# Optimization experiments

Hardware: AMD Instinct MI355X
Metric: run time of the kernel (lower is better)

## Reference

```python
import jax, jax.numpy as jnp
import numpy as np

B, S, D, H = 2, 2048, 1024, 16
DK = D // H


def setup_inputs() -> dict:
    key = jax.random.key(0)
    ks = jax.random.split(key, 11)
    scale = 1.0 / np.sqrt(D)
    inp = {
        "query": jax.random.normal(ks[0], (B, S, D), dtype=jnp.float32),
        "key": jax.random.normal(ks[1], (B, S, D), dtype=jnp.float32),
        "value": jax.random.normal(ks[2], (B, S, D), dtype=jnp.float32),
        "Wq": jax.random.normal(ks[3], (D, D), dtype=jnp.float32) * scale,
        "bq": jnp.zeros((D,), dtype=jnp.float32),
        "Wk": jax.random.normal(ks[4], (D, D), dtype=jnp.float32) * scale,
        "bk": jnp.zeros((D,), dtype=jnp.float32),
        "Wv": jax.random.normal(ks[5], (D, D), dtype=jnp.float32) * scale,
        "bv": jnp.zeros((D,), dtype=jnp.float32),
        "Wo": jax.random.normal(ks[6], (D, D), dtype=jnp.float32) * scale,
        "bo": jnp.zeros((D,), dtype=jnp.float32),
    }
    return inp


def _split_heads(x):
    # [B,S,D] -> [B,H,S,DK]
    b, s, _ = x.shape
    return x.reshape(b, s, H, DK).transpose(0, 2, 1, 3)


def reference(query, key, value, Wq, bq, Wk, bk, Wv, bv, Wo, bo):
    q = _split_heads(query @ Wq.T + bq)
    k = _split_heads(key @ Wk.T + bk)
    v = _split_heads(value @ Wv.T + bv)
    # scaled dot-product attention: [B,H,S,S]
    scores = jnp.einsum("bhqd,bhkd->bhqk", q, k) / np.sqrt(DK).astype(np.float32)
    attn = jax.nn.softmax(scores, axis=-1)  # stable max-subtract softmax, same math
    ctx = jnp.einsum("bhqk,bhkd->bhqd", attn, v)  # [B,H,S,DK]
    ctx = ctx.transpose(0, 2, 1, 3).reshape(query.shape[0], -1, H * DK)
    return ctx @ Wo.T + bo
```

## Files before the change

### kernel.cpp

```cpp
#include <hip/hip_runtime.h>
#include <math.h>

constexpr int NB = 2;
constexpr int NS = 2048;
constexpr int ND = 1024;
constexpr int NH = 16;
constexpr int NDK = 64;

typedef __attribute__((ext_vector_type(8))) short short8;
typedef __attribute__((ext_vector_type(4))) float floatx4;

__device__ inline unsigned short f2bf(float x) {
    unsigned u = __builtin_bit_cast(unsigned, x);
    u += 0x7fffu + ((u >> 16) & 1u);
    return (unsigned short)(u >> 16);
}

#define GLOAD_LDS16(g, l) __builtin_amdgcn_global_load_lds( \
    (const __attribute__((address_space(1))) void*)(g),     \
    (__attribute__((address_space(3))) void*)(l), 16, 0, 0)

#define QSCALE 0.18033688f

__global__ __launch_bounds__(256) void cvt_all(
    const float* __restrict__ s0, const float* __restrict__ s1,
    const float* __restrict__ s2, const float* __restrict__ s3,
    const float* __restrict__ s4, const float* __restrict__ s5,
    const float* __restrict__ s6,
    unsigned short* __restrict__ d0, unsigned short* __restrict__ d1,
    unsigned short* __restrict__ d2, unsigned short* __restrict__ d3,
    unsigned short* __restrict__ d4, unsigned short* __restrict__ d5,
    unsigned short* __restrict__ d6)
{
    const int y = blockIdx.y;
    const float* srcs[7] = {s0, s1, s2, s3, s4, s5, s6};
    unsigned short* dsts[7] = {d0, d1, d2, d3, d4, d5, d6};
    const int nel = (y < 3) ? NB * NS * ND : ND * ND;
    int i = (blockIdx.x * 256 + threadIdx.x) * 8;
    if (i >= nel) return;
    const float* s = srcs[y];
    unsigned short* d = dsts[y];
    float4 a = *(const float4*)(s + i);
    float4 b = *(const float4*)(s + i + 4);
    unsigned short t[8] = {f2bf(a.x), f2bf(a.y), f2bf(a.z), f2bf(a.w),
                           f2bf(b.x), f2bf(b.y), f2bf(b.z), f2bf(b.w)};
    *(uint4*)(d + i) = *(uint4*)t;
}

__global__ __launch_bounds__(256) void gemm_qkv(
    const unsigned short* __restrict__ Xq, const unsigned short* __restrict__ Xk,
    const unsigned short* __restrict__ Xv,
    const unsigned short* __restrict__ Wq, const unsigned short* __restrict__ Wk,
    const unsigned short* __restrict__ Wv,
    const float* __restrict__ bq, const float* __restrict__ bk,
    const float* __restrict__ bv,
    unsigned short* __restrict__ Cq, unsigned short* __restrict__ Ck,
    unsigned short* __restrict__ Cv)
{
    __shared__ unsigned short As[128 * 32];
    __shared__ unsigned short Bs[128 * 32];
    const int tid = threadIdx.x, w = tid >> 6, lane = tid & 63;
    const int lo = lane & 15, quad = lane >> 4;
    const int bid = blockIdx.x;
    const int seg = bid >> 8;
    const int wi  = bid & 255;
    const int K = ND;

    int bm, bn;
    const unsigned short *A, *Bw;
    const float* bias;
    if (seg == 2)      { bn = wi & 31; bm = wi >> 5; A = Wv; Bw = Xv; bias = bv; }
    else if (seg == 1) { bn = wi & 7;  bm = wi >> 3; A = Xk; Bw = Wk; bias = bk; }
    else               { bn = wi & 7;  bm = wi >> 3; A = Xq; Bw = Wq; bias = bq; }

    const int wm = (w >> 1) * 64, wn = (w & 1) * 64;

    const int srow = tid >> 2;
    const int sch = (tid & 3) ^ (srow & 3);
    const unsigned short* Ag0 = A + (size_t)(bm * 128 + srow) * K + sch * 8;
    const unsigned short* Ag1 = Ag0 + (size_t)64 * K;
    const unsigned short* Bg0 = Bw + (size_t)(bn * 128 + srow) * K + sch * 8;
    const unsigned short* Bg1 = Bg0 + (size_t)64 * K;
    unsigned short* AsD0 = As + tid * 8;
    unsigned short* AsD1 = As + (tid + 256) * 8;
    unsigned short* BsD0 = Bs + tid * 8;
    unsigned short* BsD1 = Bs + (tid + 256) * 8;

    floatx4 acc[4][4];
    #pragma unroll
    for (int i = 0; i < 4; ++i)
        #pragma unroll
        for (int j = 0; j < 4; ++j) acc[i][j] = (floatx4){0.f, 0.f, 0.f, 0.f};

    const int rpos = (quad ^ (lo & 3)) * 8;

    for (int k0 = 0; k0 < K; k0 += 32) {
        GLOAD_LDS16(Ag0 + k0, AsD0);
        GLOAD_LDS16(Ag1 + k0, AsD1);
        GLOAD_LDS16(Bg0 + k0, BsD0);
        GLOAD_LDS16(Bg1 + k0, BsD1);
        __syncthreads();

        short8 af[4], bf[4];
        #pragma unroll
        for (int i = 0; i < 4; ++i)
            af[i] = *(const short8*)(As + (wm + i * 16 + lo) * 32 + rpos);
        #pragma unroll
        for (int j = 0; j < 4; ++j)
            bf[j] = *(const short8*)(Bs + (wn + j * 16 + lo) * 32 + rpos);

        #pragma unroll
        for (int i = 0; i < 4; ++i)
            #pragma unroll
            for (int j = 0; j < 4; ++j)
                acc[i][j] = __builtin_amdgcn_mfma_f32_16x16x32_bf16(af[i], bf[j], acc[i][j], 0, 0, 0);
        __syncthreads();
    }

    if (seg < 2) {
        unsigned short* C = seg ? Ck : Cq;
        const float scale = seg ? 1.f : QSCALE;
        #pragma unroll
        for (int j = 0; j < 4; ++j) {
            const int col = bn * 128 + wn + j * 16 + lo;
            const float bb = bias[col];
            #pragma unroll
            for (int i = 0; i < 4; ++i)
                #pragma unroll
                for (int r = 0; r < 4; ++r) {
                    const int row = bm * 128 + wm + i * 16 + quad * 4 + r;
                    C[(size_t)row * ND + col] = f2bf((acc[i][j][r] + bb) * scale);
                }
        }
    } else {
        #pragma unroll
        for (int i = 0; i < 4; ++i)
            #pragma unroll
            for (int r = 0; r < 4; ++r) {
                const int row = bm * 128 + wm + i * 16 + quad * 4 + r;
                const float bb = bias[row];
                #pragma unroll
                for (int j = 0; j < 4; ++j) {
                    const int col = bn * 128 + wn + j * 16 + lo;
                    const int b = col >> 11, s = col & (NS - 1);
                    Cv[(size_t)(b * ND + row) * NS + s] = f2bf(acc[i][j][r] + bb);
                }
            }
    }
}

__global__ __launch_bounds__(256) void gemm_o(
    const unsigned short* __restrict__ A, const unsigned short* __restrict__ Bw,
    const float* __restrict__ bias, float* __restrict__ Cout)
{
    __shared__ unsigned short As[64 * 64];
    __shared__ unsigned short Bs[128 * 64];
    const int tid = threadIdx.x, w = tid >> 6, lane = tid & 63;
    const int lo = lane & 15, quad = lane >> 4;
    const int bn = blockIdx.x, bm = blockIdx.y;
    const int K = ND;
    const int wm = (w >> 1) * 32, wn = (w & 1) * 64;

    const int ar0 = tid >> 3,            ag0 = (tid & 7) ^ (ar0 & 7);
    const int ar1 = (tid + 256) >> 3,    ag1 = (tid & 7) ^ (ar1 & 7);
    const unsigned short* Ag0 = A + (size_t)(bm * 64 + ar0) * K + ag0 * 8;
    const unsigned short* Ag1 = A + (size_t)(bm * 64 + ar1) * K + ag1 * 8;
    unsigned short* AsD0 = As + tid * 8;
    unsigned short* AsD1 = As + (tid + 256) * 8;

    const unsigned short* Bg[4];
    unsigned short* BsD[4];
    #pragma unroll
    for (int p = 0; p < 4; ++p) {
        int c = tid + 256 * p, r = c >> 3, g = (c & 7) ^ (r & 7);
        Bg[p] = Bw + (size_t)(bn * 128 + r) * K + g * 8;
        BsD[p] = Bs + c * 8;
    }

    floatx4 acc[2][4];
    #pragma unroll
    for (int i = 0; i < 2; ++i)
        #pragma unroll
        for (int j = 0; j < 4; ++j) acc[i][j] = (floatx4){0.f, 0.f, 0.f, 0.f};

    for (int k0 = 0; k0 < K; k0 += 64) {
        GLOAD_LDS16(Ag0 + k0, AsD0);
        GLOAD_LDS16(Ag1 + k0, AsD1);
        #pragma unroll
        for (int p = 0; p < 4; ++p) GLOAD_LDS16(Bg[p] + k0, BsD[p]);
        __syncthreads();

        #pragma unroll
        for (int s = 0; s < 2; ++s) {
            const int pos = ((s * 4 + quad) ^ (lo & 7)) * 8;
            short8 af[2], bf[4];
            #pragma unroll
            for (int i = 0; i < 2; ++i)
                af[i] = *(const short8*)(As + (wm + i * 16 + lo) * 64 + pos);
            #pragma unroll
            for (int j = 0; j < 4; ++j)
                bf[j] = *(const short8*)(Bs + (wn + j * 16 + lo) * 64 + pos);
            #pragma unroll
            for (int i = 0; i < 2; ++i)
                #pragma unroll
                for (int j = 0; j < 4; ++j)
                    acc[i][j] = __builtin_amdgcn_mfma_f32_16x16x32_bf16(af[i], bf[j], acc[i][j], 0, 0, 0);
        }
        __syncthreads();
    }

    #pragma unroll
    for (int j = 0; j < 4; ++j) {
        const int col = bn * 128 + wn + j * 16 + lo;
        const float bb = bias[col];
        #pragma unroll
        for (int i = 0; i < 2; ++i)
            #pragma unroll
            for (int r = 0; r < 4; ++r) {
                const int row = bm * 64 + wm + i * 16 + quad * 4 + r;
                Cout[(size_t)row * ND + col] = acc[i][j][r] + bb;
            }
    }
}

constexpr int PRS = 72;

__global__ __launch_bounds__(256, 4) void attn_mfma(
    const unsigned short* __restrict__ qb,
    const unsigned short* __restrict__ kb,
    const unsigned short* __restrict__ vt,
    float* __restrict__ cacc0, float* __restrict__ cacc1,
    float* __restrict__ lbuf)
{
    __shared__ unsigned short Ks[64 * 64];
    __shared__ unsigned short Vs[64 * 64];
    __shared__ unsigned short Pt[4][32 * PRS];

    const int tid = threadIdx.x, w = tid >> 6, lane = tid & 63;
    const int lo = lane & 15, quad = lane >> 4;
    const int qgrp = blockIdx.x;
    const int ksp  = blockIdx.y;
    const int bh   = blockIdx.z;
    const int b = bh >> 4, h = bh & 15;
    const int q0 = qgrp * 128 + w * 32;

    short8 qf[2][2];
    #pragma unroll
    for (int qt = 0; qt < 2; ++qt) {
        const unsigned short* qrow =
            qb + (size_t)(b * NS + q0 + qt * 16 + lo) * ND + h * NDK + quad * 8;
        qf[qt][0] = *(const short8*)(qrow);
        qf[qt][1] = *(const short8*)(qrow + 32);
    }

    const int c0 = tid, c1 = tid + 256;
    const int r0 = c0 >> 3, g0 = (c0 & 7) ^ (r0 & 7);
    const int r1 = c1 >> 3, g1 = (c1 & 7) ^ (r1 & 7);
    const unsigned short* Ksrc0 = kb + (size_t)(b * NS + r0) * ND + h * NDK + g0 * 8;
    const unsigned short* Ksrc1 = kb + (size_t)(b * NS + r1) * ND + h * NDK + g1 * 8;
    const unsigned short* Vsrc0 = vt + (size_t)(bh * NDK + r0) * NS + g0 * 8;
    const unsigned short* Vsrc1 = vt + (size_t)(bh * NDK + r1) * NS + g1 * 8;
    unsigned short* Kd0 = Ks + c0 * 8;
    unsigned short* Kd1 = Ks + c1 * 8;
    unsigned short* Vd0 = Vs + c0 * 8;
    unsigned short* Vd1 = Vs + c1 * 8;

    floatx4 acc[2][4], lacc[2];
    #pragma unroll
    for (int qt = 0; qt < 2; ++qt) {
        lacc[qt] = (floatx4){0.f, 0.f, 0.f, 0.f};
        #pragma unroll
        for (int cb = 0; cb < 4; ++cb) acc[qt][cb] = (floatx4){0.f, 0.f, 0.f, 0.f};
    }

    const short8 ones = {0x3F80, 0x3F80, 0x3F80, 0x3F80,
                         0x3F80, 0x3F80, 0x3F80, 0x3F80};
    unsigned short* pw = &Pt[w][0];
    const int pos0 = (quad ^ (lo & 7)) * 8;
    const int pos1 = ((4 + quad) ^ (lo & 7)) * 8;

    for (int key0 = ksp * 1024; key0 < ksp * 1024 + 1024; key0 += 64) {
        GLOAD_LDS16(Ksrc0 + (size_t)key0 * ND, Kd0);
        GLOAD_LDS16(Ksrc1 + (size_t)key0 * ND, Kd1);
        GLOAD_LDS16(Vsrc0 + key0, Vd0);
        GLOAD_LDS16(Vsrc1 + key0, Vd1);
        __syncthreads();

        floatx4 s[2][4];
        #pragma unroll
        for (int t = 0; t < 4; ++t) {
            const int rw = (t * 16 + lo) * 64;
            const short8 kf0 = *(const short8*)(Ks + rw + pos0);
            const short8 kf1 = *(const short8*)(Ks + rw + pos1);
            #pragma unroll
            for (int qt = 0; qt < 2; ++qt) {
                s[qt][t] = __builtin_amdgcn_mfma_f32_16x16x32_bf16(
                    kf0, qf[qt][0], (floatx4){0.f, 0.f, 0.f, 0.f}, 0, 0, 0);
                s[qt][t] = __builtin_amdgcn_mfma_f32_16x16x32_bf16(
                    kf1, qf[qt][1], s[qt][t], 0, 0, 0);
            }
        }

        #pragma unroll
        for (int qt = 0; qt < 2; ++qt)
            #pragma unroll
            for (int t = 0; t < 4; ++t) {
                unsigned u0 = __builtin_bit_cast(unsigned, __builtin_amdgcn_exp2f(s[qt][t][0]));
                unsigned u1 = __builtin_bit_cast(unsigned, __builtin_amdgcn_exp2f(s[qt][t][1]));
                unsigned u2 = __builtin_bit_cast(unsigned, __builtin_amdgcn_exp2f(s[qt][t][2]));
                unsigned u3 = __builtin_bit_cast(unsigned, __builtin_amdgcn_exp2f(s[qt][t][3]));
                uint2 pk = {(u0 >> 16) | (u1 & 0xFFFF0000u),
                            (u2 >> 16) | (u3 & 0xFFFF0000u)};
                *(uint2*)(pw + (qt * 16 + lo) * PRS + t * 16 + quad * 4) = pk;
            }

        short8 pf[2][2];
        #pragma unroll
        for (int qt = 0; qt < 2; ++qt) {
            pf[qt][0] = *(const short8*)(pw + (qt * 16 + lo) * PRS + quad * 8);
            pf[qt][1] = *(const short8*)(pw + (qt * 16 + lo) * PRS + 32 + quad * 8);
            lacc[qt] = __builtin_amdgcn_mfma_f32_16x16x32_bf16(pf[qt][0], ones, lacc[qt], 0, 0, 0);
            lacc[qt] = __builtin_amdgcn_mfma_f32_16x16x32_bf16(pf[qt][1], ones, lacc[qt], 0, 0, 0);
        }

        #pragma unroll
        for (int cb = 0; cb < 4; ++cb) {
            const int rw = (cb * 16 + lo) * 64;
            const short8 vf0 = *(const short8*)(Vs + rw + pos0);
            const short8 vf1 = *(const short8*)(Vs + rw + pos1);
            #pragma unroll
            for (int qt = 0; qt < 2; ++qt) {
                acc[qt][cb] = __builtin_amdgcn_mfma_f32_16x16x32_bf16(pf[qt][0], vf0, acc[qt][cb], 0, 0, 0);
                acc[qt][cb] = __builtin_amdgcn_mfma_f32_16x16x32_bf16(pf[qt][1], vf1, acc[qt][cb], 0, 0, 0);
            }
        }
        __syncthreads();
    }

    float* ca = ksp ? cacc1 : cacc0;
    float* lb = lbuf + (size_t)ksp * (NB * NH * NS);
    #pragma unroll
    for (int qt = 0; qt < 2; ++qt) {
        #pragma unroll
        for (int cb = 0; cb < 4; ++cb)
            #pragma unroll
            for (int r = 0; r < 4; ++r) {
                size_t off = (size_t)(b * NS + q0 + qt * 16 + quad * 4 + r) * ND
                           + h * NDK + cb * 16 + lo;
                ca[off] = acc[qt][cb][r];
            }
        if (lo == 0)
            #pragma unroll
            for (int r = 0; r < 4; ++r)
                lb[(size_t)bh * NS + q0 + qt * 16 + quad * 4 + r] = lacc[qt][r];
    }
}

__global__ __launch_bounds__(256) void divide_ctx(
    const float* __restrict__ cacc0, const float* __restrict__ cacc1,
    const float* __restrict__ lbuf, unsigned short* __restrict__ ctx)
{
    int idx = blockIdx.x * 256 + threadIdx.x;
    int base = idx * 8;
    int row = base >> 10;
    int col = base & 1023;
    int b = row >> 11, sq = row & 2047, h = col >> 6;
    size_t li = (size_t)((b << 4) + h) * NS + sq;
    float inv = 1.f / (lbuf[li] + lbuf[li + (size_t)NB * NH * NS]);
    float4 a0 = *(const float4*)(cacc0 + base);
    float4 a1 = *(const float4*)(cacc0 + base + 4);
    float4 c0 = *(const float4*)(cacc1 + base);
    float4 c1 = *(const float4*)(cacc1 + base + 4);
    unsigned short o[8] = {
        f2bf((a0.x + c0.x) * inv), f2bf((a0.y + c0.y) * inv),
        f2bf((a0.z + c0.z) * inv), f2bf((a0.w + c0.w) * inv),
        f2bf((a1.x + c1.x) * inv), f2bf((a1.y + c1.y) * inv),
        f2bf((a1.z + c1.z) * inv), f2bf((a1.w + c1.w) * inv)};
    *(uint4*)(ctx + base) = *(uint4*)o;
}

extern "C" void kernel_launch(void* const* d_in, const int* in_sizes, int n_in,
                              void* d_out, int out_size, void* d_ws, size_t ws_size,
                              hipStream_t stream)
{
    const float* query = (const float*)d_in[0];
    const float* key   = (const float*)d_in[1];
    const float* value = (const float*)d_in[2];
    const float* Wq    = (const float*)d_in[3];
    const float* bq    = (const float*)d_in[4];
    const float* Wk    = (const float*)d_in[5];
    const float* bk    = (const float*)d_in[6];
    const float* Wv    = (const float*)d_in[7];
    const float* bv    = (const float*)d_in[8];
    const float* Wo    = (const float*)d_in[9];
    const float* bo    = (const float*)d_in[10];
    float* out = (float*)d_out;

    const size_t n  = (size_t)NB * NS * ND;
    const size_t nw = (size_t)ND * ND;

    unsigned short* X0   = (unsigned short*)d_ws;
    unsigned short* X1   = X0 + n;
    unsigned short* X2   = X1 + n;
    unsigned short* W0   = X2 + n;
    unsigned short* W1   = W0 + nw;
    unsigned short* W2   = W1 + nw;
    unsigned short* W3   = W2 + nw;
    unsigned short* qbuf = W3 + nw;
    unsigned short* kbuf = qbuf + n;
    unsigned short* vtb  = kbuf + n;
    float* cacc1 = (float*)(vtb + n);
    float* lbuf  = cacc1 + n;
    float* cacc0 = (float*)X1;
    unsigned short* ctxb = qbuf;

    const int M = NB * NS;

    cvt_all<<<dim3((int)(n / 2048), 7), 256, 0, stream>>>(
        query, key, value, Wq, Wk, Wv, Wo, X0, X1, X2, W0, W1, W2, W3);

    gemm_qkv<<<768, 256, 0, stream>>>(X0, X1, X2, W0, W1, W2,
                                      bq, bk, bv, qbuf, kbuf, vtb);

    attn_mfma<<<dim3(NS / 128, 2, NB * NH), 256, 0, stream>>>(
        qbuf, kbuf, vtb, cacc0, cacc1, lbuf);

    divide_ctx<<<(int)(n / 8 / 256), 256, 0, stream>>>(cacc0, cacc1, lbuf, ctxb);

    gemm_o<<<dim3(ND / 128, M / 64), 256, 0, stream>>>(ctxb, W3, bo, out);
}
```

Baseline: 234.4 us.

## Fuse fp32-to-bf16 conversion into GEMMs and fold context normalization into output GEMM

Removes the standalone conversion kernel by having the QKV and output GEMMs load fp32 operands through registers and convert to bf16 when writing to shared memory, using a register prefetch of the next K tile. It also removes the divide_ctx kernel: the output GEMM now reads both split-K context partials and the softmax denominators directly, sums and normalizes them, then converts to bf16 on the fly. This cuts two launches and the intermediate bf16 round trips through global memory. In exchange the GEMMs read twice as many bytes per tile, and the output GEMM re-reads the partials once per column block. The async global-to-LDS loads are replaced by register staging, which adds VALU work and register pressure.

```diff
diff --git a/kernel.cpp b/kernel.cpp
--- a/kernel.cpp
+++ b/kernel.cpp
@@ -16,42 +16,23 @@
     return (unsigned short)(u >> 16);
 }
 
+__device__ inline uint4 pack8(float4 a, float4 b) {
+    unsigned short t[8] = {f2bf(a.x), f2bf(a.y), f2bf(a.z), f2bf(a.w),
+                           f2bf(b.x), f2bf(b.y), f2bf(b.z), f2bf(b.w)};
+    return *(uint4*)t;
+}
+
 #define GLOAD_LDS16(g, l) __builtin_amdgcn_global_load_lds( \
     (const __attribute__((address_space(1))) void*)(g),     \
     (__attribute__((address_space(3))) void*)(l), 16, 0, 0)
 
 #define QSCALE 0.18033688f
 
-__global__ __launch_bounds__(256) void cvt_all(
-    const float* __restrict__ s0, const float* __restrict__ s1,
-    const float* __restrict__ s2, const float* __restrict__ s3,
-    const float* __restrict__ s4, const float* __restrict__ s5,
-    const float* __restrict__ s6,
-    unsigned short* __restrict__ d0, unsigned short* __restrict__ d1,
-    unsigned short* __restrict__ d2, unsigned short* __restrict__ d3,
-    unsigned short* __restrict__ d4, unsigned short* __restrict__ d5,
-    unsigned short* __restrict__ d6)
-{
-    const int y = blockIdx.y;
-    const float* srcs[7] = {s0, s1, s2, s3, s4, s5, s6};
-    unsigned short* dsts[7] = {d0, d1, d2, d3, d4, d5, d6};
-    const int nel = (y < 3) ? NB * NS * ND : ND * ND;
-    int i = (blockIdx.x * 256 + threadIdx.x) * 8;
-    if (i >= nel) return;
-    const float* s = srcs[y];
-    unsigned short* d = dsts[y];
-    float4 a = *(const float4*)(s + i);
-    float4 b = *(const float4*)(s + i + 4);
-    unsigned short t[8] = {f2bf(a.x), f2bf(a.y), f2bf(a.z), f2bf(a.w),
-                           f2bf(b.x), f2bf(b.y), f2bf(b.z), f2bf(b.w)};
-    *(uint4*)(d + i) = *(uint4*)t;
-}
-
 __global__ __launch_bounds__(256) void gemm_qkv(
-    const unsigned short* __restrict__ Xq, const unsigned short* __restrict__ Xk,
-    const unsigned short* __restrict__ Xv,
-    const unsigned short* __restrict__ Wq, const unsigned short* __restrict__ Wk,
-    const unsigned short* __restrict__ Wv,
+    const float* __restrict__ Xq, const float* __restrict__ Xk,
+    const float* __restrict__ Xv,
+    const float* __restrict__ Wq, const float* __restrict__ Wk,
+    const float* __restrict__ Wv,
     const float* __restrict__ bq, const float* __restrict__ bk,
     const float* __restrict__ bv,
     unsigned short* __restrict__ Cq, unsigned short* __restrict__ Ck,
@@ -67,8 +48,7 @@
     const int K = ND;
 
     int bm, bn;
-    const unsigned short *A, *Bw;
-    const float* bias;
+    const float *A, *Bw, *bias;
     if (seg == 2)      { bn = wi & 31; bm = wi >> 5; A = Wv; Bw = Xv; bias = bv; }
     else if (seg == 1) { bn = wi & 7;  bm = wi >> 3; A = Xk; Bw = Wk; bias = bk; }
     else               { bn = wi & 7;  bm = wi >> 3; A = Xq; Bw = Wq; bias = bq; }
@@ -77,10 +57,10 @@
 
     const int srow = tid >> 2;
     const int sch = (tid & 3) ^ (srow & 3);
-    const unsigned short* Ag0 = A + (size_t)(bm * 128 + srow) * K + sch * 8;
-    const unsigned short* Ag1 = Ag0 + (size_t)64 * K;
-    const unsigned short* Bg0 = Bw + (size_t)(bn * 128 + srow) * K + sch * 8;
-    const unsigned short* Bg1 = Bg0 + (size_t)64 * K;
+    const float* Ag0 = A + (size_t)(bm * 128 + srow) * K + sch * 8;
+    const float* Ag1 = Ag0 + (size_t)64 * K;
+    const float* Bg0 = Bw + (size_t)(bn * 128 + srow) * K + sch * 8;
+    const float* Bg1 = Bg0 + (size_t)64 * K;
     unsigned short* AsD0 = As + tid * 8;
     unsigned short* AsD1 = As + (tid + 256) * 8;
     unsigned short* BsD0 = Bs + tid * 8;
@@ -94,12 +74,27 @@
 
     const int rpos = (quad ^ (lo & 3)) * 8;
 
+    float4 ra[4], rb[4];
+    ra[0] = *(const float4*)(Ag0);     ra[1] = *(const float4*)(Ag0 + 4);
+    ra[2] = *(const float4*)(Ag1);     ra[3] = *(const float4*)(Ag1 + 4);
+    rb[0] = *(const float4*)(Bg0);     rb[1] = *(const float4*)(Bg0 + 4);
+    rb[2] = *(const float4*)(Bg1);     rb[3] = *(const float4*)(Bg1 + 4);
+
     for (int k0 = 0; k0 < K; k0 += 32) {
-        GLOAD_LDS16(Ag0 + k0, AsD0);
-        GLOAD_LDS16(Ag1 + k0, AsD1);
-        GLOAD_LDS16(Bg0 + k0, BsD0);
-        GLOAD_LDS16(Bg1 + k0, BsD1);
-        __syncthreads();
+        __syncthreads();
+        *(uint4*)AsD0 = pack8(ra[0], ra[1]);
+        *(uint4*)AsD1 = pack8(ra[2], ra[3]);
+        *(uint4*)BsD0 = pack8(rb[0], rb[1]);
+        *(uint4*)BsD1 = pack8(rb[2], rb[3]);
+        __syncthreads();
+
+        const int kn = k0 + 32;
+        if (kn < K) {
+            ra[0] = *(const float4*)(Ag0 + kn); ra[1] = *(const float4*)(Ag0 + kn + 4);
+            ra[2] = *(const float4*)(Ag1 + kn); ra[3] = *(const float4*)(Ag1 + kn + 4);
+            rb[0] = *(const float4*)(Bg0 + kn); rb[1] = *(const float4*)(Bg0 + kn + 4);
+            rb[2] = *(const float4*)(Bg1 + kn); rb[3] = *(const float4*)(Bg1 + kn + 4);
+        }
 
         short8 af[4], bf[4];
         #pragma unroll
@@ -114,7 +109,6 @@
             #pragma unroll
             for (int j = 0; j < 4; ++j)
                 acc[i][j] = __builtin_amdgcn_mfma_f32_16x16x32_bf16(af[i], bf[j], acc[i][j], 0, 0, 0);
-        __syncthreads();
     }
 
     if (seg < 2) {
@@ -145,80 +139,6 @@
                     const int b = col >> 11, s = col & (NS - 1);
                     Cv[(size_t)(b * ND + row) * NS + s] = f2bf(acc[i][j][r] + bb);
                 }
-            }
-    }
-}
-
-__global__ __launch_bounds__(256) void gemm_o(
-    const unsigned short* __restrict__ A, const unsigned short* __restrict__ Bw,
-    const float* __restrict__ bias, float* __restrict__ Cout)
-{
-    __shared__ unsigned short As[64 * 64];
-    __shared__ unsigned short Bs[128 * 64];
-    const int tid = threadIdx.x, w = tid >> 6, lane = tid & 63;
-    const int lo = lane & 15, quad = lane >> 4;
-    const int bn = blockIdx.x, bm = blockIdx.y;
-    const int K = ND;
-    const int wm = (w >> 1) * 32, wn = (w & 1) * 64;
-
-    const int ar0 = tid >> 3,            ag0 = (tid & 7) ^ (ar0 & 7);
-    const int ar1 = (tid + 256) >> 3,    ag1 = (tid & 7) ^ (ar1 & 7);
-    const unsigned short* Ag0 = A + (size_t)(bm * 64 + ar0) * K + ag0 * 8;
-    const unsigned short* Ag1 = A + (size_t)(bm * 64 + ar1) * K + ag1 * 8;
-    unsigned short* AsD0 = As + tid * 8;
-    unsigned short* AsD1 = As + (tid + 256) * 8;
-
-    const unsigned short* Bg[4];
-    unsigned short* BsD[4];
-    #pragma unroll
-    for (int p = 0; p < 4; ++p) {
-        int c = tid + 256 * p, r = c >> 3, g = (c & 7) ^ (r & 7);
-        Bg[p] = Bw + (size_t)(bn * 128 + r) * K + g * 8;
-        BsD[p] = Bs + c * 8;
-    }
-
-    floatx4 acc[2][4];
-    #pragma unroll
-    for (int i = 0; i < 2; ++i)
-        #pragma unroll
-        for (int j = 0; j < 4; ++j) acc[i][j] = (floatx4){0.f, 0.f, 0.f, 0.f};
-
-    for (int k0 = 0; k0 < K; k0 += 64) {
-        GLOAD_LDS16(Ag0 + k0, AsD0);
-        GLOAD_LDS16(Ag1 + k0, AsD1);
-        #pragma unroll
-        for (int p = 0; p < 4; ++p) GLOAD_LDS16(Bg[p] + k0, BsD[p]);
-        __syncthreads();
-
-        #pragma unroll
-        for (int s = 0; s < 2; ++s) {
-            const int pos = ((s * 4 + quad) ^ (lo & 7)) * 8;
-            short8 af[2], bf[4];
-            #pragma unroll
-            for (int i = 0; i < 2; ++i)
-                af[i] = *(const short8*)(As + (wm + i * 16 + lo) * 64 + pos);
-            #pragma unroll
-            for (int j = 0; j < 4; ++j)
-                bf[j] = *(const short8*)(Bs + (wn + j * 16 + lo) * 64 + pos);
-            #pragma unroll
-            for (int i = 0; i < 2; ++i)
-                #pragma unroll
-                for (int j = 0; j < 4; ++j)
-                    acc[i][j] = __builtin_amdgcn_mfma_f32_16x16x32_bf16(af[i], bf[j], acc[i][j], 0, 0, 0);
-        }
-        __syncthreads();
-    }
-
-    #pragma unroll
-    for (int j = 0; j < 4; ++j) {
-        const int col = bn * 128 + wn + j * 16 + lo;
-        const float bb = bias[col];
-        #pragma unroll
-        for (int i = 0; i < 2; ++i)
-            #pragma unroll
-            for (int r = 0; r < 4; ++r) {
-                const int row = bm * 64 + wm + i * 16 + quad * 4 + r;
-                Cout[(size_t)row * ND + col] = acc[i][j][r] + bb;
             }
     }
 }
@@ -356,27 +276,130 @@
     }
 }
 
-__global__ __launch_bounds__(256) void divide_ctx(
+__global__ __launch_bounds__(256) void gemm_o(
     const float* __restrict__ cacc0, const float* __restrict__ cacc1,
-    const float* __restrict__ lbuf, unsigned short* __restrict__ ctx)
+    const float* __restrict__ lbuf, const float* __restrict__ Bw,
+    const float* __restrict__ bias, float* __restrict__ Cout)
 {
-    int idx = blockIdx.x * 256 + threadIdx.x;
-    int base = idx * 8;
-    int row = base >> 10;
-    int col = base & 1023;
-    int b = row >> 11, sq = row & 2047, h = col >> 6;
-    size_t li = (size_t)((b << 4) + h) * NS + sq;
-    float inv = 1.f / (lbuf[li] + lbuf[li + (size_t)NB * NH * NS]);
-    float4 a0 = *(const float4*)(cacc0 + base);
-    float4 a1 = *(const float4*)(cacc0 + base + 4);
-    float4 c0 = *(const float4*)(cacc1 + base);
-    float4 c1 = *(const float4*)(cacc1 + base + 4);
-    unsigned short o[8] = {
-        f2bf((a0.x + c0.x) * inv), f2bf((a0.y + c0.y) * inv),
-        f2bf((a0.z + c0.z) * inv), f2bf((a0.w + c0.w) * inv),
-        f2bf((a1.x + c1.x) * inv), f2bf((a1.y + c1.y) * inv),
-        f2bf((a1.z + c1.z) * inv), f2bf((a1.w + c1.w) * inv)};
-    *(uint4*)(ctx + base) = *(uint4*)o;
+    __shared__ unsigned short As[64 * 64];
+    __shared__ unsigned short Bs[128 * 64];
+    const int tid = threadIdx.x, w = tid >> 6, lane = tid & 63;
+    const int lo = lane & 15, quad = lane >> 4;
+    const int bn = blockIdx.x, bm = blockIdx.y;
+    const int K = ND;
+    const int wm = (w >> 1) * 32, wn = (w & 1) * 64;
+    const size_t LHALF = (size_t)NB * NH * NS;
+
+    const int ar = tid >> 3;
+    const int ag = (tid & 7) ^ (ar & 7);
+    const int tok0 = bm * 64 + ar, tok1 = tok0 + 32;
+    const float* A00 = cacc0 + (size_t)tok0 * ND + ag * 8;
+    const float* A01 = cacc1 + (size_t)tok0 * ND + ag * 8;
+    const float* A10 = cacc0 + (size_t)tok1 * ND + ag * 8;
+    const float* A11 = cacc1 + (size_t)tok1 * ND + ag * 8;
+    const size_t lb0 = (size_t)((tok0 >> 11) << 4) * NS + (tok0 & (NS - 1));
+    const size_t lb1 = (size_t)((tok1 >> 11) << 4) * NS + (tok1 & (NS - 1));
+    unsigned short* AsD0 = As + tid * 8;
+    unsigned short* AsD1 = As + (tid + 256) * 8;
+
+    const float* Bg[4];
+    unsigned short* BsD[4];
+    #pragma unroll
+    for (int p = 0; p < 4; ++p) {
+        int c = tid + 256 * p, r = c >> 3, g = (c & 7) ^ (r & 7);
+        Bg[p] = Bw + (size_t)(bn * 128 + r) * K + g * 8;
+        BsD[p] = Bs + c * 8;
+    }
+
+    floatx4 acc[2][4];
+    #pragma unroll
+    for (int i = 0; i < 2; ++i)
+        #pragma unroll
+        for (int j = 0; j < 4; ++j) acc[i][j] = (floatx4){0.f, 0.f, 0.f, 0.f};
+
+    float4 ra[8], rb[8];
+    float lv0, lv1;
+    {
+        ra[0] = *(const float4*)(A00);     ra[1] = *(const float4*)(A00 + 4);
+        ra[2] = *(const float4*)(A01);     ra[3] = *(const float4*)(A01 + 4);
+        ra[4] = *(const float4*)(A10);     ra[5] = *(const float4*)(A10 + 4);
+        ra[6] = *(const float4*)(A11);     ra[7] = *(const float4*)(A11 + 4);
+        #pragma unroll
+        for (int p = 0; p < 4; ++p) {
+            rb[2 * p]     = *(const float4*)(Bg[p]);
+            rb[2 * p + 1] = *(const float4*)(Bg[p] + 4);
+        }
+        lv0 = lbuf[lb0] + lbuf[lb0 + LHALF];
+        lv1 = lbuf[lb1] + lbuf[lb1 + LHALF];
+    }
+
+    for (int k0 = 0; k0 < K; k0 += 64) {
+        const float inv0 = __builtin_amdgcn_rcpf(lv0);
+        const float inv1 = __builtin_amdgcn_rcpf(lv1);
+        __syncthreads();
+        {
+            float4 s0 = {(ra[0].x + ra[2].x) * inv0, (ra[0].y + ra[2].y) * inv0,
+                         (ra[0].z + ra[2].z) * inv0, (ra[0].w + ra[2].w) * inv0};
+            float4 s1 = {(ra[1].x + ra[3].x) * inv0, (ra[1].y + ra[3].y) * inv0,
+                         (ra[1].z + ra[3].z) * inv0, (ra[1].w + ra[3].w) * inv0};
+            *(uint4*)AsD0 = pack8(s0, s1);
+            float4 s2 = {(ra[4].x + ra[6].x) * inv1, (ra[4].y + ra[6].y) * inv1,
+                         (ra[4].z + ra[6].z) * inv1, (ra[4].w + ra[6].w) * inv1};
+            float4 s3 = {(ra[5].x + ra[7].x) * inv1, (ra[5].y + ra[7].y) * inv1,
+                         (ra[5].z + ra[7].z) * inv1, (ra[5].w + ra[7].w) * inv1};
+            *(uint4*)AsD1 = pack8(s2, s3);
+        }
+        #pragma unroll
+        for (int p = 0; p < 4; ++p)
+            *(uint4*)BsD[p] = pack8(rb[2 * p], rb[2 * p + 1]);
+        __syncthreads();
+
+        const int kn = k0 + 64;
+        if (kn < K) {
+            ra[0] = *(const float4*)(A00 + kn); ra[1] = *(const float4*)(A00 + kn + 4);
+            ra[2] = *(const float4*)(A01 + kn); ra[3] = *(const float4*)(A01 + kn + 4);
+            ra[4] = *(const float4*)(A10 + kn); ra[5] = *(const float4*)(A10 + kn + 4);
+            ra[6] = *(const float4*)(A11 + kn); ra[7] = *(const float4*)(A11 + kn + 4);
+            #pragma unroll
+            for (int p = 0; p < 4; ++p) {
+                rb[2 * p]     = *(const float4*)(Bg[p] + kn);
+                rb[2 * p + 1] = *(const float4*)(Bg[p] + kn + 4);
+            }
+            const size_t hoff = (size_t)(kn >> 6) * NS;
+            lv0 = lbuf[lb0 + hoff] + lbuf[lb0 + hoff + LHALF];
+            lv1 = lbuf[lb1 + hoff] + lbuf[lb1 + hoff + LHALF];
+        }
+
+        #pragma unroll
+        for (int s = 0; s < 2; ++s) {
+            const int pos = ((s * 4 + quad) ^ (lo & 7)) * 8;
+            short8 af[2], bf[4];
+            #pragma unroll
+            for (int i = 0; i < 2; ++i)
+                af[i] = *(const short8*)(As + (wm + i * 16 + lo) * 64 + pos);
+            #pragma unroll
+            for (int j = 0; j < 4; ++j)
+                bf[j] = *(const short8*)(Bs + (wn + j * 16 + lo) * 64 + pos);
+            #pragma unroll
+            for (int i = 0; i < 2; ++i)
+                #pragma unroll
+                for (int j = 0; j < 4; ++j)
+                    acc[i][j] = __builtin_amdgcn_mfma_f32_16x16x32_bf16(af[i], bf[j], acc[i][j], 0, 0, 0);
+        }
+    }
+
+    #pragma unroll
+    for (int j = 0; j < 4; ++j) {
+        const int col = bn * 128 + wn + j * 16 + lo;
+        const float bb = bias[col];
+        #pragma unroll
+        for (int i = 0; i < 2; ++i)
+            #pragma unroll
+            for (int r = 0; r < 4; ++r) {
+                const int row = bm * 64 + wm + i * 16 + quad * 4 + r;
+                Cout[(size_t)row * ND + col] = acc[i][j][r] + bb;
+            }
+    }
 }
 
 extern "C" void kernel_launch(void* const* d_in, const int* in_sizes, int n_in,
@@ -396,36 +419,23 @@
     const float* bo    = (const float*)d_in[10];
     float* out = (float*)d_out;
 
-    const size_t n  = (size_t)NB * NS * ND;
-    const size_t nw = (size_t)ND * ND;
-
-    unsigned short* X0   = (unsigned short*)d_ws;
-    unsigned short* X1   = X0 + n;
-    unsigned short* X2   = X1 + n;
-    unsigned short* W0   = X2 + n;
-    unsigned short* W1   = W0 + nw;
-    unsigned short* W2   = W1 + nw;
-    unsigned short* W3   = W2 + nw;
-    unsigned short* qbuf = W3 + nw;
+    const size_t n = (size_t)NB * NS * ND;
+
+    unsigned short* qbuf = (unsigned short*)d_ws;
     unsigned short* kbuf = qbuf + n;
     unsigned short* vtb  = kbuf + n;
-    float* cacc1 = (float*)(vtb + n);
+    float* cacc0 = (float*)(vtb + n);
+    float* cacc1 = cacc0 + n;
     float* lbuf  = cacc1 + n;
-    float* cacc0 = (float*)X1;
-    unsigned short* ctxb = qbuf;
 
     const int M = NB * NS;
 
-    cvt_all<<<dim3((int)(n / 2048), 7), 256, 0, stream>>>(
-        query, key, value, Wq, Wk, Wv, Wo, X0, X1, X2, W0, W1, W2, W3);
-
-    gemm_qkv<<<768, 256, 0, stream>>>(X0, X1, X2, W0, W1, W2,
+    gemm_qkv<<<768, 256, 0, stream>>>(query, key, value, Wq, Wk, Wv,
                                       bq, bk, bv, qbuf, kbuf, vtb);
 
     attn_mfma<<<dim3(NS / 128, 2, NB * NH), 256, 0, stream>>>(
         qbuf, kbuf, vtb, cacc0, cacc1, lbuf);
 
-    divide_ctx<<<(int)(n / 8 / 256), 256, 0, stream>>>(cacc0, cacc1, lbuf, ctxb);
-
-    gemm_o<<<dim3(ND / 128, M / 64), 256, 0, stream>>>(ctxb, W3, bo, out);
-}
+    gemm_o<<<dim3(ND / 128, M / 64), 256, 0, stream>>>(
+        cacc0, cacc1, lbuf, Wo, bo, out);
+}
```

Result: slower. 269.1 us (+14.8%).

## Fuse context normalization into output GEMM and remap blocks for XCD locality

Applied to the files above, without the earlier changes.

Removes the divide_ctx kernel. The output projection GEMM now reads the two fp32 split-K partial contexts and the softmax denominators directly, normalizes them, converts to bf16 and stages the result into LDS. These register loads are prefetched one K-step ahead. Separately, block indices in the QKV GEMM, attention and output GEMM are remapped so that blocks landing on the same XCD share operand tiles, aiming for better L2 reuse. This saves one launch and a bf16 round trip, but the output GEMM now reads fp32 A data (twice the bytes, two buffers) and converts it once per N-tile.

```diff
diff --git a/kernel.cpp b/kernel.cpp
--- a/kernel.cpp
+++ b/kernel.cpp
@@ -14,6 +14,12 @@
     unsigned u = __builtin_bit_cast(unsigned, x);
     u += 0x7fffu + ((u >> 16) & 1u);
     return (unsigned short)(u >> 16);
+}
+
+__device__ inline uint4 pack8(float4 a, float4 b) {
+    unsigned short t[8] = {f2bf(a.x), f2bf(a.y), f2bf(a.z), f2bf(a.w),
+                           f2bf(b.x), f2bf(b.y), f2bf(b.z), f2bf(b.w)};
+    return *(uint4*)t;
 }
 
 #define GLOAD_LDS16(g, l) __builtin_amdgcn_global_load_lds( \
@@ -42,9 +48,7 @@
     unsigned short* d = dsts[y];
     float4 a = *(const float4*)(s + i);
     float4 b = *(const float4*)(s + i + 4);
-    unsigned short t[8] = {f2bf(a.x), f2bf(a.y), f2bf(a.z), f2bf(a.w),
-                           f2bf(b.x), f2bf(b.y), f2bf(b.z), f2bf(b.w)};
-    *(uint4*)(d + i) = *(uint4*)t;
+    *(uint4*)(d + i) = pack8(a, b);
 }
 
 __global__ __launch_bounds__(256) void gemm_qkv(
@@ -64,14 +68,21 @@
     const int bid = blockIdx.x;
     const int seg = bid >> 8;
     const int wi  = bid & 255;
+    const int xcd = wi & 7;
+    const int t   = wi >> 3;
     const int K = ND;
 
     int bm, bn;
     const unsigned short *A, *Bw;
     const float* bias;
-    if (seg == 2)      { bn = wi & 31; bm = wi >> 5; A = Wv; Bw = Xv; bias = bv; }
-    else if (seg == 1) { bn = wi & 7;  bm = wi >> 3; A = Xk; Bw = Wk; bias = bk; }
-    else               { bn = wi & 7;  bm = wi >> 3; A = Xq; Bw = Wq; bias = bq; }
+    if (seg == 2) {
+        bm = t & 7; bn = (t >> 3) * 8 + xcd;
+        A = Wv; Bw = Xv; bias = bv;
+    } else {
+        bn = t & 7; bm = (t >> 3) * 8 + xcd;
+        if (seg == 1) { A = Xk; Bw = Wk; bias = bk; }
+        else          { A = Xq; Bw = Wq; bias = bq; }
+    }
 
     const int wm = (w >> 1) * 64, wn = (w & 1) * 64;
 
@@ -149,80 +160,6 @@
     }
 }
 
-__global__ __launch_bounds__(256) void gemm_o(
-    const unsigned short* __restrict__ A, const unsigned short* __restrict__ Bw,
-    const float* __restrict__ bias, float* __restrict__ Cout)
-{
-    __shared__ unsigned short As[64 * 64];
-    __shared__ unsigned short Bs[128 * 64];
-    const int tid = threadIdx.x, w = tid >> 6, lane = tid & 63;
-    const int lo = lane & 15, quad = lane >> 4;
-    const int bn = blockIdx.x, bm = blockIdx.y;
-    const int K = ND;
-    const int wm = (w >> 1) * 32, wn = (w & 1) * 64;
-
-    const int ar0 = tid >> 3,            ag0 = (tid & 7) ^ (ar0 & 7);
-    const int ar1 = (tid + 256) >> 3,    ag1 = (tid & 7) ^ (ar1 & 7);
-    const unsigned short* Ag0 = A + (size_t)(bm * 64 + ar0) * K + ag0 * 8;
-    const unsigned short* Ag1 = A + (size_t)(bm * 64 + ar1) * K + ag1 * 8;
-    unsigned short* AsD0 = As + tid * 8;
-    unsigned short* AsD1 = As + (tid + 256) * 8;
-
-    const unsigned short* Bg[4];
-    unsigned short* BsD[4];
-    #pragma unroll
-    for (int p = 0; p < 4; ++p) {
-        int c = tid + 256 * p, r = c >> 3, g = (c & 7) ^ (r & 7);
-        Bg[p] = Bw + (size_t)(bn * 128 + r) * K + g * 8;
-        BsD[p] = Bs + c * 8;
-    }
-
-    floatx4 acc[2][4];
-    #pragma unroll
-    for (int i = 0; i < 2; ++i)
-        #pragma unroll
-        for (int j = 0; j < 4; ++j) acc[i][j] = (floatx4){0.f, 0.f, 0.f, 0.f};
-
-    for (int k0 = 0; k0 < K; k0 += 64) {
-        GLOAD_LDS16(Ag0 + k0, AsD0);
-        GLOAD_LDS16(Ag1 + k0, AsD1);
-        #pragma unroll
-        for (int p = 0; p < 4; ++p) GLOAD_LDS16(Bg[p] + k0, BsD[p]);
-        __syncthreads();
-
-        #pragma unroll
-        for (int s = 0; s < 2; ++s) {
-            const int pos = ((s * 4 + quad) ^ (lo & 7)) * 8;
-            short8 af[2], bf[4];
-            #pragma unroll
-            for (int i = 0; i < 2; ++i)
-                af[i] = *(const short8*)(As + (wm + i * 16 + lo) * 64 + pos);
-            #pragma unroll
-            for (int j = 0; j < 4; ++j)
-                bf[j] = *(const short8*)(Bs + (wn + j * 16 + lo) * 64 + pos);
-            #pragma unroll
-            for (int i = 0; i < 2; ++i)
-                #pragma unroll
-                for (int j = 0; j < 4; ++j)
-                    acc[i][j] = __builtin_amdgcn_mfma_f32_16x16x32_bf16(af[i], bf[j], acc[i][j], 0, 0, 0);
-        }
-        __syncthreads();
-    }
-
-    #pragma unroll
-    for (int j = 0; j < 4; ++j) {
-        const int col = bn * 128 + wn + j * 16 + lo;
-        const float bb = bias[col];
-        #pragma unroll
-        for (int i = 0; i < 2; ++i)
-            #pragma unroll
-            for (int r = 0; r < 4; ++r) {
-                const int row = bm * 64 + wm + i * 16 + quad * 4 + r;
-                Cout[(size_t)row * ND + col] = acc[i][j][r] + bb;
-            }
-    }
-}
-
 constexpr int PRS = 72;
 
 __global__ __launch_bounds__(256, 4) void attn_mfma(
@@ -238,9 +175,12 @@
 
     const int tid = threadIdx.x, w = tid >> 6, lane = tid & 63;
     const int lo = lane & 15, quad = lane >> 4;
-    const int qgrp = blockIdx.x;
-    const int ksp  = blockIdx.y;
-    const int bh   = blockIdx.z;
+    const int bid = blockIdx.x;
+    const int xcd = bid & 7;
+    const int tt  = bid >> 3;
+    const int qgrp = tt & 15;
+    const int bhk  = (tt >> 4) * 8 + xcd;
+    const int bh = bhk >> 1, ksp = bhk & 1;
     const int b = bh >> 4, h = bh & 15;
     const int q0 = qgrp * 128 + w * 32;
 
@@ -356,27 +296,121 @@
     }
 }
 
-__global__ __launch_bounds__(256) void divide_ctx(
+__global__ __launch_bounds__(256) void gemm_o(
     const float* __restrict__ cacc0, const float* __restrict__ cacc1,
-    const float* __restrict__ lbuf, unsigned short* __restrict__ ctx)
+    const float* __restrict__ lbuf, const unsigned short* __restrict__ Bw,
+    const float* __restrict__ bias, float* __restrict__ Cout)
 {
-    int idx = blockIdx.x * 256 + threadIdx.x;
-    int base = idx * 8;
-    int row = base >> 10;
-    int col = base & 1023;
-    int b = row >> 11, sq = row & 2047, h = col >> 6;
-    size_t li = (size_t)((b << 4) + h) * NS + sq;
-    float inv = 1.f / (lbuf[li] + lbuf[li + (size_t)NB * NH * NS]);
-    float4 a0 = *(const float4*)(cacc0 + base);
-    float4 a1 = *(const float4*)(cacc0 + base + 4);
-    float4 c0 = *(const float4*)(cacc1 + base);
-    float4 c1 = *(const float4*)(cacc1 + base + 4);
-    unsigned short o[8] = {
-        f2bf((a0.x + c0.x) * inv), f2bf((a0.y + c0.y) * inv),
-        f2bf((a0.z + c0.z) * inv), f2bf((a0.w + c0.w) * inv),
-        f2bf((a1.x + c1.x) * inv), f2bf((a1.y + c1.y) * inv),
-        f2bf((a1.z + c1.z) * inv), f2bf((a1.w + c1.w) * inv)};
-    *(uint4*)(ctx + base) = *(uint4*)o;
+    __shared__ unsigned short As[64 * 64];
+    __shared__ unsigned short Bs[128 * 64];
+    const int tid = threadIdx.x, w = tid >> 6, lane = tid & 63;
+    const int lo = lane & 15, quad = lane >> 4;
+    const int bid = blockIdx.x;
+    const int xcd = bid & 7;
+    const int tt  = bid >> 3;
+    const int bn  = tt & 7;
+    const int bm  = (tt >> 3) * 8 + xcd;
+    const int K = ND;
+    const int wm = (w >> 1) * 32, wn = (w & 1) * 64;
+    const size_t LHALF = (size_t)NB * NH * NS;
+
+    const int ar = tid >> 3;
+    const int ag = (tid & 7) ^ (ar & 7);
+    const int tok0 = bm * 64 + ar, tok1 = tok0 + 32;
+    const float* A00 = cacc0 + (size_t)tok0 * ND + ag * 8;
+    const float* A01 = cacc1 + (size_t)tok0 * ND + ag * 8;
+    const float* A10 = cacc0 + (size_t)tok1 * ND + ag * 8;
+    const float* A11 = cacc1 + (size_t)tok1 * ND + ag * 8;
+    const size_t lb0 = (size_t)((tok0 >> 11) << 4) * NS + (tok0 & (NS - 1));
+    const size_t lb1 = (size_t)((tok1 >> 11) << 4) * NS + (tok1 & (NS - 1));
+    unsigned short* AsD0 = As + tid * 8;
+    unsigned short* AsD1 = As + (tid + 256) * 8;
+
+    const unsigned short* Bg[4];
+    unsigned short* BsD[4];
+    #pragma unroll
+    for (int p = 0; p < 4; ++p) {
+        int c = tid + 256 * p, r = c >> 3, g = (c & 7) ^ (r & 7);
+        Bg[p] = Bw + (size_t)(bn * 128 + r) * K + g * 8;
+        BsD[p] = Bs + c * 8;
+    }
+
+    floatx4 acc[2][4];
+    #pragma unroll
+    for (int i = 0; i < 2; ++i)
+        #pragma unroll
+        for (int j = 0; j < 4; ++j) acc[i][j] = (floatx4){0.f, 0.f, 0.f, 0.f};
+
+    float4 ra[8];
+    float lv0, lv1;
+    ra[0] = *(const float4*)(A00);     ra[1] = *(const float4*)(A00 + 4);
+    ra[2] = *(const float4*)(A01);     ra[3] = *(const float4*)(A01 + 4);
+    ra[4] = *(const float4*)(A10);     ra[5] = *(const float4*)(A10 + 4);
+    ra[6] = *(const float4*)(A11);     ra[7] = *(const float4*)(A11 + 4);
+    lv0 = lbuf[lb0] + lbuf[lb0 + LHALF];
+    lv1 = lbuf[lb1] + lbuf[lb1 + LHALF];
+
+    for (int k0 = 0; k0 < K; k0 += 64) {
+        const float inv0 = __builtin_amdgcn_rcpf(lv0);
+        const float inv1 = __builtin_amdgcn_rcpf(lv1);
+        __syncthreads();
+        #pragma unroll
+        for (int p = 0; p < 4; ++p) GLOAD_LDS16(Bg[p] + k0, BsD[p]);
+        {
+            float4 s0 = {(ra[0].x + ra[2].x) * inv0, (ra[0].y + ra[2].y) * inv0,
+                         (ra[0].z + ra[2].z) * inv0, (ra[0].w + ra[2].w) * inv0};
+            float4 s1 = {(ra[1].x + ra[3].x) * inv0, (ra[1].y + ra[3].y) * inv0,
+                         (ra[1].z + ra[3].z) * inv0, (ra[1].w + ra[3].w) * inv0};
+            *(uint4*)AsD0 = pack8(s0, s1);
+            float4 s2 = {(ra[4].x + ra[6].x) * inv1, (ra[4].y + ra[6].y) * inv1,
+                         (ra[4].z + ra[6].z) * inv1, (ra[4].w + ra[6].w) * inv1};
+            float4 s3 = {(ra[5].x + ra[7].x) * inv1, (ra[5].y + ra[7].y) * inv1,
+                         (ra[5].z + ra[7].z) * inv1, (ra[5].w + ra[7].w) * inv1};
+            *(uint4*)AsD1 = pack8(s2, s3);
+        }
+        __syncthreads();
+
+        const int kn = k0 + 64;
+        if (kn < K) {
+            ra[0] = *(const float4*)(A00 + kn); ra[1] = *(const float4*)(A00 + kn + 4);
+            ra[2] = *(const float4*)(A01 + kn); ra[3] = *(const float4*)(A01 + kn + 4);
+            ra[4] = *(const float4*)(A10 + kn); ra[5] = *(const float4*)(A10 + kn + 4);
+            ra[6] = *(const float4*)(A11 + kn); ra[7] = *(const float4*)(A11 + kn + 4);
+            const size_t hoff = (size_t)(kn >> 6) * NS;
+            lv0 = lbuf[lb0 + hoff] + lbuf[lb0 + hoff + LHALF];
+            lv1 = lbuf[lb1 + hoff] + lbuf[lb1 + hoff + LHALF];
+        }
+
+        #pragma unroll
+        for (int s = 0; s < 2; ++s) {
+            const int pos = ((s * 4 + quad) ^ (lo & 7)) * 8;
+            short8 af[2], bf[4];
+            #pragma unroll
+            for (int i = 0; i < 2; ++i)
+                af[i] = *(const short8*)(As + (wm + i * 16 + lo) * 64 + pos);
+            #pragma unroll
+            for (int j = 0; j < 4; ++j)
+                bf[j] = *(const short8*)(Bs + (wn + j * 16 + lo) * 64 + pos);
+            #pragma unroll
+            for (int i = 0; i < 2; ++i)
+                #pragma unroll
+                for (int j = 0; j < 4; ++j)
+                    acc[i][j] = __builtin_amdgcn_mfma_f32_16x16x32_bf16(af[i], bf[j], acc[i][j], 0, 0, 0);
+        }
+    }
+
+    #pragma unroll
+    for (int j = 0; j < 4; ++j) {
+        const int col = bn * 128 + wn + j * 16 + lo;
+        const float bb = bias[col];
+        #pragma unroll
+        for (int i = 0; i < 2; ++i)
+            #pragma unroll
+            for (int r = 0; r < 4; ++r) {
+                const int row = bm * 64 + wm + i * 16 + quad * 4 + r;
+                Cout[(size_t)row * ND + col] = acc[i][j][r] + bb;
+            }
+    }
 }
 
 extern "C" void kernel_launch(void* const* d_in, const int* in_sizes, int n_in,
@@ -412,7 +446,6 @@
     float* cacc1 = (float*)(vtb + n);
     float* lbuf  = cacc1 + n;
     float* cacc0 = (float*)X1;
-    unsigned short* ctxb = qbuf;
 
     const int M = NB * NS;
 
@@ -422,10 +455,7 @@
     gemm_qkv<<<768, 256, 0, stream>>>(X0, X1, X2, W0, W1, W2,
                                       bq, bk, bv, qbuf, kbuf, vtb);
 
-    attn_mfma<<<dim3(NS / 128, 2, NB * NH), 256, 0, stream>>>(
-        qbuf, kbuf, vtb, cacc0, cacc1, lbuf);
-
-    divide_ctx<<<(int)(n / 8 / 256), 256, 0, stream>>>(cacc0, cacc1, lbuf, ctxb);
-
-    gemm_o<<<dim3(ND / 128, M / 64), 256, 0, stream>>>(ctxb, W3, bo, out);
-}
+    attn_mfma<<<1024, 256, 0, stream>>>(qbuf, kbuf, vtb, cacc0, cacc1, lbuf);
+
+    gemm_o<<<512, 256, 0, stream>>>(cacc0, cacc1, lbuf, W3, bo, out);
+}
```

Measured after the change: 233.1 us. Within noise of the previous version (-0.6%).
